# Kernel optimization log

Measured on AMD Instinct MI355X. Metric: run time of the kernel, lower is better.

The kernel has to match this reference:

```python
import jax, jax.numpy as jnp
import numpy as np

B, N, DIM = 8, 16384, 256
DIM_HEAD, NUM_HEADS = 64, 8
D = DIM_HEAD * NUM_HEADS  # 512
SCALE = DIM_HEAD ** (-0.5)


def setup_inputs() -> dict:
    key = jax.random.key(0)
    ks = jax.random.split(key, 11)
    s = 0.02
    return {
        "x": jax.random.normal(ks[0], (B, N, DIM), dtype=jnp.float32),
        "Wq": jax.random.normal(ks[1], (DIM, D), dtype=jnp.float32) * s,
        "bq": jax.random.normal(ks[2], (D,), dtype=jnp.float32) * s,
        "Wk": jax.random.normal(ks[3], (DIM, D), dtype=jnp.float32) * s,
        "bk": jax.random.normal(ks[4], (D,), dtype=jnp.float32) * s,
        "qw": jax.random.normal(ks[5], (D, 1), dtype=jnp.float32),  # query_weight parameter
        "Wp": jax.random.normal(ks[6], (D, D), dtype=jnp.float32) * s,
        "bp": jax.random.normal(ks[7], (D,), dtype=jnp.float32) * s,
        "Wo": jax.random.normal(ks[8], (D, DIM_HEAD), dtype=jnp.float32) * s,
        "bo": jax.random.normal(ks[9], (DIM_HEAD,), dtype=jnp.float32) * s,
    }


def reference(x, Wq, bq, Wk, bk, qw, Wp, bp, Wo, bo):
    # query, key: [B, N, D]
    query = jnp.einsum("bnc,cd->bnd", x, Wq) + bq
    key = jnp.einsum("bnc,cd->bnd", x, Wk) + bk
    # per-token scalar score: [B, N, 1]
    score = (query @ qw) * SCALE
    # global attention context: sum over sequence axis -> [B, 1, D]
    attn_weight = jnp.sum(score * query, axis=1, keepdims=True)
    # broadcast (repeat over N), gate keys, project, residual add of query
    out = jnp.einsum("bnd,de->bne", attn_weight * key, Wp) + bp + query
    # output projection D -> dim_head: [B, N, DIM_HEAD]
    out = jnp.einsum("bnd,dh->bnh", out, Wo) + bo
    return out
```

## Files before the change

### kernel.cpp

```cpp
#include <hip/hip_runtime.h>
#include <hip/hip_bf16.h>


#define NN 16384
#define CC 256
#define DD 512
#define HH 64
#define SCALE_F 0.125f

#define OFF_SX    0
#define OFF_TSUM  2048
#define OFF_WQQ   2056
#define OFF_BQQ   2312
#define OFF_WPWO  2320
#define OFF_WQWO  35088
#define OFF_CBIAS 51472
#define OFF_BEFF  51536
#define OFF_WEFFT 52048

typedef unsigned short ushort_t;
typedef __attribute__((ext_vector_type(8))) short short8;
typedef __attribute__((ext_vector_type(4))) float floatx4;

__device__ __forceinline__ unsigned short f2bf(float f) {
    __hip_bfloat16 h = __float2bfloat16(f);
    return __builtin_bit_cast(unsigned short, h);
}

__global__ __launch_bounds__(256) void k_prep(
    const float* __restrict__ Wq, const float* __restrict__ bq,
    const float* __restrict__ qw, const float* __restrict__ Wp,
    const float* __restrict__ bp, const float* __restrict__ Wo,
    const float* __restrict__ bo, float* __restrict__ ws)
{
    __shared__ float lds[2056];
    const int tid = threadIdx.x;
    const int bid = blockIdx.x;

    if (bid < 128) {
        const int d0 = bid * 4;
        for (int i = tid; i < 2048; i += 256) lds[i] = Wp[d0 * 512 + i];
        __syncthreads();
        const int dl = tid >> 6, h = tid & 63;
        float acc = 0.f;
        for (int e = 0; e < 512; ++e)
            acc = fmaf(lds[dl * 512 + e], Wo[e * 64 + h], acc);
        ws[OFF_WPWO + (d0 + dl) * 64 + h] = acc;
    } else if (bid < 192) {
        const int c0 = (bid - 128) * 4;
        for (int i = tid; i < 2048; i += 256) lds[i] = Wq[c0 * 512 + i];
        __syncthreads();
        const int cl = tid >> 6, h = tid & 63;
        float acc = 0.f;
        for (int e = 0; e < 512; ++e)
            acc = fmaf(lds[cl * 512 + e], Wo[e * 64 + h], acc);
        ws[OFF_WQWO + (c0 + cl) * 64 + h] = acc;
    } else if (bid == 192) {
        float* lb = lds + 2048;
        for (int i = tid; i < 512; i += 256) lds[i] = qw[i];
        if (tid == 0) *lb = 0.f;
        __syncthreads();
        const float* wr = Wq + tid * 512;
        float acc = 0.f;
        for (int d = 0; d < 512; ++d) acc = fmaf(wr[d], lds[d], acc);
        ws[OFF_WQQ + tid] = acc;
        float pb = fmaf(bq[tid], lds[tid], bq[tid + 256] * lds[tid + 256]);
#pragma unroll
        for (int m = 1; m < 64; m <<= 1) pb += __shfl_xor(pb, m);
        if ((tid & 63) == 0) atomicAdd(lb, pb);
        __syncthreads();
        if (tid == 0) ws[OFF_BQQ] = *lb;
    } else if (bid == 193) {
        const int h = tid & 63, part = tid >> 6;
        float acc = 0.f;
        for (int d = part * 128; d < part * 128 + 128; ++d)
            acc = fmaf(bq[d] + bp[d], Wo[d * 64 + h], acc);
        lds[part * 64 + h] = acc;
        __syncthreads();
        if (tid < 64)
            ws[OFF_CBIAS + tid] = bo[tid] + lds[tid] + lds[64 + tid] +
                                  lds[128 + tid] + lds[192 + tid];
    } else {
        for (int i = tid; i < 2056; i += 256) ws[OFF_SX + i] = 0.f;
    }
}

__global__ __launch_bounds__(256) void k_phase1(
    const float* __restrict__ x, float* __restrict__ ws)
{
    const int tid  = threadIdx.x;
    const int lane = tid & 63;
    const int wave = tid >> 6;
    const int quad = lane >> 4;
    const int l15  = lane & 15;
    __shared__ float lacc[256];
    __shared__ float ltsum;

    floatx4 wv[4];
#pragma unroll
    for (int j = 0; j < 4; ++j)
        wv[j] = *(const floatx4*)(ws + OFF_WQQ + j * 64 + l15 * 4);
    const float bqq = ws[OFF_BQQ];

    const int vb = blockIdx.x;
    const int b = vb >> 7;
    const int rbase = (vb & 127) * 128;
    lacc[tid] = 0.f;
    if (tid == 0) ltsum = 0.f;
    __syncthreads();

    const float* xb = x + (size_t)b * NN * CC;
    const int r0 = rbase + wave * 32 + quad;
    floatx4 accs[4];
#pragma unroll
    for (int j = 0; j < 4; ++j)
#pragma unroll
        for (int k = 0; k < 4; ++k) accs[j][k] = 0.f;
    float ts = 0.f;

#pragma unroll 2
    for (int it = 0; it < 8; ++it) {
        const float* xr = xb + (size_t)(r0 + it * 4) * CC + l15 * 4;
        const floatx4 x0 = *(const floatx4*)(xr);
        const floatx4 x1 = *(const floatx4*)(xr + 64);
        const floatx4 x2 = *(const floatx4*)(xr + 128);
        const floatx4 x3 = *(const floatx4*)(xr + 192);
        float p = 0.f;
#pragma unroll
        for (int k = 0; k < 4; ++k) {
            p = fmaf(x0[k], wv[0][k], p);
            p = fmaf(x1[k], wv[1][k], p);
            p = fmaf(x2[k], wv[2][k], p);
            p = fmaf(x3[k], wv[3][k], p);
        }
        p += __shfl_xor(p, 1);
        p += __shfl_xor(p, 2);
        p += __shfl_xor(p, 4);
        p += __shfl_xor(p, 8);
        const float t = SCALE_F * (p + bqq);
        ts += t;
#pragma unroll
        for (int k = 0; k < 4; ++k) {
            accs[0][k] = fmaf(t, x0[k], accs[0][k]);
            accs[1][k] = fmaf(t, x1[k], accs[1][k]);
            accs[2][k] = fmaf(t, x2[k], accs[2][k]);
            accs[3][k] = fmaf(t, x3[k], accs[3][k]);
        }
    }

#pragma unroll
    for (int j = 0; j < 4; ++j)
#pragma unroll
        for (int k = 0; k < 4; ++k) {
            float v = accs[j][k];
            v += __shfl_xor(v, 16);
            v += __shfl_xor(v, 32);
            if (quad == 0) atomicAdd(&lacc[j * 64 + l15 * 4 + k], v);
        }
    if (l15 == 0) atomicAdd(&ltsum, ts);
    __syncthreads();
    atomicAdd(&ws[OFF_SX + b * 256 + tid], lacc[tid]);
    if (tid == 0) atomicAdd(&ws[OFF_TSUM + b], ltsum);
}

__global__ __launch_bounds__(256) void k_weff(
    const float* __restrict__ Wq, const float* __restrict__ bq,
    const float* __restrict__ Wk, const float* __restrict__ bk,
    float* __restrict__ ws)
{
    const int tid = threadIdx.x;
    const int vb = blockIdx.x;
    const int b = vb >> 3;
    const int c0 = (vb & 7) * 32;
    __shared__ float lsx[256];
    __shared__ float law[512];
    __shared__ float lts;
    __shared__ float wpT[64 * 64];

    lsx[tid] = ws[OFF_SX + b * 256 + tid];
    if (tid == 0) lts = ws[OFF_TSUM + b];
    __syncthreads();
    const float tsum = lts;

    for (int d = tid; d < 512; d += 256) {
        float acc = tsum * bq[d];
        for (int c = 0; c < 256; ++c) acc = fmaf(lsx[c], Wq[c * 512 + d], acc);
        law[d] = acc;
    }
    __syncthreads();

    const int c = c0 + (tid >> 3);
    const int hb = (tid & 7) * 8;
    float acc[8];
#pragma unroll
    for (int j = 0; j < 8; ++j) acc[j] = ws[OFF_WQWO + c * 64 + hb + j];

    for (int t8 = 0; t8 < 8; ++t8) {
        const int d0 = t8 * 64;
        for (int i = tid; i < 4096; i += 256) wpT[i] = ws[OFF_WPWO + d0 * 64 + i];
        __syncthreads();
        for (int dl = 0; dl < 64; ++dl) {
            const float g = Wk[c * 512 + d0 + dl] * law[d0 + dl];
            const floatx4 p0 = *(const floatx4*)(wpT + dl * 64 + hb);
            const floatx4 p1 = *(const floatx4*)(wpT + dl * 64 + hb + 4);
            acc[0] = fmaf(g, p0[0], acc[0]); acc[1] = fmaf(g, p0[1], acc[1]);
            acc[2] = fmaf(g, p0[2], acc[2]); acc[3] = fmaf(g, p0[3], acc[3]);
            acc[4] = fmaf(g, p1[0], acc[4]); acc[5] = fmaf(g, p1[1], acc[5]);
            acc[6] = fmaf(g, p1[2], acc[6]); acc[7] = fmaf(g, p1[3], acc[7]);
        }
        __syncthreads();
    }

    ushort_t* wt = (ushort_t*)(ws + OFF_WEFFT) + (size_t)b * (HH * CC);
#pragma unroll
    for (int j = 0; j < 8; ++j)
        wt[(size_t)(hb + j) * CC + c] = f2bf(acc[j]);

    if ((vb & 7) == 0 && tid < 64) {
        float a = ws[OFF_CBIAS + tid];
        for (int d = 0; d < 512; ++d)
            a = fmaf(bk[d] * law[d], ws[OFF_WPWO + d * 64 + tid], a);
        ws[OFF_BEFF + b * 64 + tid] = a;
    }
}

__global__ __launch_bounds__(256) void k_out(
    const float* __restrict__ x, const float* __restrict__ ws,
    float* __restrict__ out)
{
    const int tid  = threadIdx.x;
    const int lane = tid & 63;
    const int wave = tid >> 6;
    const int quad = lane >> 4;
    const int l15  = lane & 15;
    __shared__ __align__(16) ushort_t lwt[64 * 264];

    const int vb = blockIdx.x;
    const int b = vb >> 7;
    const int rt0 = vb & 127;
    const ushort_t* wt = (const ushort_t*)(ws + OFF_WEFFT) + (size_t)b * (HH * CC);
    for (int o = tid; o < 2048; o += 256) {
        const int h = o >> 5, seg = o & 31;
        *(short8*)(lwt + h * 264 + seg * 8) = *(const short8*)(wt + h * 256 + seg * 8);
    }
    __syncthreads();

    const float* beff = ws + OFF_BEFF + b * 64;
    float bias[4];
#pragma unroll
    for (int ht = 0; ht < 4; ++ht) bias[ht] = beff[ht * 16 + l15];

#pragma unroll
    for (int s = 0; s < 2; ++s) {
        const int row0 = (rt0 + s * 128) * 64 + wave * 16;
        const float* xr = x + ((size_t)b * NN + row0 + l15) * CC + quad * 8;
        short8 afrag[8];
#pragma unroll
        for (int kk = 0; kk < 8; ++kk) {
            const floatx4 u0 = *(const floatx4*)(xr + kk * 32);
            const floatx4 u1 = *(const floatx4*)(xr + kk * 32 + 4);
            short8 t;
            t[0] = (short)f2bf(u0[0]); t[1] = (short)f2bf(u0[1]);
            t[2] = (short)f2bf(u0[2]); t[3] = (short)f2bf(u0[3]);
            t[4] = (short)f2bf(u1[0]); t[5] = (short)f2bf(u1[1]);
            t[6] = (short)f2bf(u1[2]); t[7] = (short)f2bf(u1[3]);
            afrag[kk] = t;
        }
        floatx4 acc[4];
#pragma unroll
        for (int ht = 0; ht < 4; ++ht)
#pragma unroll
            for (int r = 0; r < 4; ++r) acc[ht][r] = 0.f;

#pragma unroll
        for (int kk = 0; kk < 8; ++kk)
#pragma unroll
            for (int ht = 0; ht < 4; ++ht) {
                const short8 bf =
                    *(const short8*)(lwt + (ht * 16 + l15) * 264 + quad * 8 + kk * 32);
                acc[ht] = __builtin_amdgcn_mfma_f32_16x16x32_bf16(
                    afrag[kk], bf, acc[ht], 0, 0, 0);
            }

#pragma unroll
        for (int ht = 0; ht < 4; ++ht) {
            const int h = ht * 16 + l15;
#pragma unroll
            for (int r = 0; r < 4; ++r) {
                const int row = row0 + quad * 4 + r;
                out[((size_t)b * NN + row) * HH + h] = acc[ht][r] + bias[ht];
            }
        }
    }
}

extern "C" void kernel_launch(void* const* d_in, const int* in_sizes, int n_in,
                              void* d_out, int out_size, void* d_ws, size_t ws_size,
                              hipStream_t stream) {
    const float* x  = (const float*)d_in[0];
    const float* Wq = (const float*)d_in[1];
    const float* bq = (const float*)d_in[2];
    const float* Wk = (const float*)d_in[3];
    const float* bk = (const float*)d_in[4];
    const float* qw = (const float*)d_in[5];
    const float* Wp = (const float*)d_in[6];
    const float* bp = (const float*)d_in[7];
    const float* Wo = (const float*)d_in[8];
    const float* bo = (const float*)d_in[9];
    float* ws  = (float*)d_ws;
    float* out = (float*)d_out;

    hipLaunchKernelGGL(k_prep,   dim3(195),  dim3(256), 0, stream,
                       Wq, bq, qw, Wp, bp, Wo, bo, ws);
    hipLaunchKernelGGL(k_phase1, dim3(1024), dim3(256), 0, stream, x, ws);
    hipLaunchKernelGGL(k_weff,   dim3(64),   dim3(256), 0, stream,
                       Wq, bq, Wk, bk, ws);
    hipLaunchKernelGGL(k_out,    dim3(1024), dim3(256), 0, stream, x, ws, out);
}
```

Baseline: 338.4 us.

## Spread effective-weight kernel across more blocks with per-thread outputs and ILP

Relaunches k_weff on a 64x8 grid where each block handles four input channels and each thread computes one output element, instead of 64 blocks each producing 32 channels via LDS-staged tiles. Inner reductions use four independent accumulators, and the bias reduction is split over four waves with an LDS combine. This raises parallelism for an under-occupied kernel. In exchange, every block recomputes the per-batch attention vector from Wq, which multiplies redundant work and L2 traffic.

```diff
diff --git a/kernel.cpp b/kernel.cpp
--- a/kernel.cpp
+++ b/kernel.cpp
@@ -169,13 +169,12 @@
     float* __restrict__ ws)
 {
     const int tid = threadIdx.x;
-    const int vb = blockIdx.x;
-    const int b = vb >> 3;
-    const int c0 = (vb & 7) * 32;
+    const int b = blockIdx.y;
+    const int c0 = blockIdx.x * 4;
     __shared__ float lsx[256];
     __shared__ float law[512];
+    __shared__ float lred[256];
     __shared__ float lts;
-    __shared__ float wpT[64 * 64];
 
     lsx[tid] = ws[OFF_SX + b * 256 + tid];
     if (tid == 0) lts = ws[OFF_TSUM + b];
@@ -183,44 +182,43 @@
     const float tsum = lts;
 
     for (int d = tid; d < 512; d += 256) {
-        float acc = tsum * bq[d];
-        for (int c = 0; c < 256; ++c) acc = fmaf(lsx[c], Wq[c * 512 + d], acc);
-        law[d] = acc;
-    }
-    __syncthreads();
-
-    const int c = c0 + (tid >> 3);
-    const int hb = (tid & 7) * 8;
-    float acc[8];
-#pragma unroll
-    for (int j = 0; j < 8; ++j) acc[j] = ws[OFF_WQWO + c * 64 + hb + j];
-
-    for (int t8 = 0; t8 < 8; ++t8) {
-        const int d0 = t8 * 64;
-        for (int i = tid; i < 4096; i += 256) wpT[i] = ws[OFF_WPWO + d0 * 64 + i];
-        __syncthreads();
-        for (int dl = 0; dl < 64; ++dl) {
-            const float g = Wk[c * 512 + d0 + dl] * law[d0 + dl];
-            const floatx4 p0 = *(const floatx4*)(wpT + dl * 64 + hb);
-            const floatx4 p1 = *(const floatx4*)(wpT + dl * 64 + hb + 4);
-            acc[0] = fmaf(g, p0[0], acc[0]); acc[1] = fmaf(g, p0[1], acc[1]);
-            acc[2] = fmaf(g, p0[2], acc[2]); acc[3] = fmaf(g, p0[3], acc[3]);
-            acc[4] = fmaf(g, p1[0], acc[4]); acc[5] = fmaf(g, p1[1], acc[5]);
-            acc[6] = fmaf(g, p1[2], acc[6]); acc[7] = fmaf(g, p1[3], acc[7]);
-        }
-        __syncthreads();
-    }
+        float a0 = 0.f, a1 = 0.f, a2 = 0.f, a3 = 0.f;
+        for (int c = 0; c < 256; c += 4) {
+            a0 = fmaf(lsx[c + 0], Wq[(c + 0) * 512 + d], a0);
+            a1 = fmaf(lsx[c + 1], Wq[(c + 1) * 512 + d], a1);
+            a2 = fmaf(lsx[c + 2], Wq[(c + 2) * 512 + d], a2);
+            a3 = fmaf(lsx[c + 3], Wq[(c + 3) * 512 + d], a3);
+        }
+        law[d] = tsum * bq[d] + ((a0 + a1) + (a2 + a3));
+    }
+    __syncthreads();
+
+    const int cl = tid >> 6, h = tid & 63;
+    const int c = c0 + cl;
+    const float* wkr = Wk + (size_t)c * 512;
+    const float* wp  = ws + OFF_WPWO;
+    float a0 = 0.f, a1 = 0.f, a2 = 0.f, a3 = 0.f;
+    for (int d = 0; d < 512; d += 4) {
+        a0 = fmaf(wkr[d + 0] * law[d + 0], wp[(d + 0) * 64 + h], a0);
+        a1 = fmaf(wkr[d + 1] * law[d + 1], wp[(d + 1) * 64 + h], a1);
+        a2 = fmaf(wkr[d + 2] * law[d + 2], wp[(d + 2) * 64 + h], a2);
+        a3 = fmaf(wkr[d + 3] * law[d + 3], wp[(d + 3) * 64 + h], a3);
+    }
+    const float acc = ws[OFF_WQWO + c * 64 + h] + ((a0 + a1) + (a2 + a3));
 
     ushort_t* wt = (ushort_t*)(ws + OFF_WEFFT) + (size_t)b * (HH * CC);
-#pragma unroll
-    for (int j = 0; j < 8; ++j)
-        wt[(size_t)(hb + j) * CC + c] = f2bf(acc[j]);
-
-    if ((vb & 7) == 0 && tid < 64) {
-        float a = ws[OFF_CBIAS + tid];
-        for (int d = 0; d < 512; ++d)
-            a = fmaf(bk[d] * law[d], ws[OFF_WPWO + d * 64 + tid], a);
-        ws[OFF_BEFF + b * 64 + tid] = a;
+    wt[(size_t)h * CC + c] = f2bf(acc);
+
+    if (blockIdx.x == 0) {
+        const int part = tid >> 6;
+        float a = 0.f;
+        for (int d = part * 128; d < part * 128 + 128; ++d)
+            a = fmaf(bk[d] * law[d], wp[d * 64 + h], a);
+        lred[tid] = a;
+        __syncthreads();
+        if (tid < 64)
+            ws[OFF_BEFF + b * 64 + tid] = ws[OFF_CBIAS + tid] + lred[tid] +
+                lred[64 + tid] + lred[128 + tid] + lred[192 + tid];
     }
 }
 
@@ -310,10 +308,10 @@
     float* ws  = (float*)d_ws;
     float* out = (float*)d_out;
 
-    hipLaunchKernelGGL(k_prep,   dim3(195),  dim3(256), 0, stream,
+    hipLaunchKernelGGL(k_prep,   dim3(195),    dim3(256), 0, stream,
                        Wq, bq, qw, Wp, bp, Wo, bo, ws);
-    hipLaunchKernelGGL(k_phase1, dim3(1024), dim3(256), 0, stream, x, ws);
-    hipLaunchKernelGGL(k_weff,   dim3(64),   dim3(256), 0, stream,
+    hipLaunchKernelGGL(k_phase1, dim3(1024),   dim3(256), 0, stream, x, ws);
+    hipLaunchKernelGGL(k_weff,   dim3(64, 8),  dim3(256), 0, stream,
                        Wq, bq, Wk, bk, ws);
-    hipLaunchKernelGGL(k_out,    dim3(1024), dim3(256), 0, stream, x, ws, out);
-}
+    hipLaunchKernelGGL(k_out,    dim3(1024),   dim3(256), 0, stream, x, ws, out);
+}
```

New measurement: 308.2 us. 1.1x faster.
